# Optimization experiments

Hardware: AMD Instinct MI355X
Metric: run time of the kernel (lower is better)

## Reference

```python
import jax, jax.numpy as jnp
import numpy as np

B, S, D_IN = 2, 2048, 1024
H, DA, DH = 16, 64, 64          # num_heads, attention_dim, head_dim (linear_hidden_dim)
EMBED = 1024
KSIZE = 1


def causal_conv1d(x_bsc, w):
    """x_bsc: (B,S,Cin); w: (Cout,Cin,K). Left-pad K-1 -> causal. Returns (B,Cout,S)."""
    k = w.shape[-1]
    x_bcs = jnp.transpose(x_bsc, (0, 2, 1))
    x_bcs = jnp.pad(x_bcs, ((0, 0), (0, 0), (k - 1, 0)))
    return jax.lax.conv_general_dilated(
        x_bcs, w, window_strides=(1,), padding='VALID',
        dimension_numbers=('NCH', 'OIH', 'NCH'))


def setup_inputs() -> dict:
    key = jax.random.key(0)
    ks = jax.random.split(key, 7)
    x = jax.random.normal(ks[0], (B, S, D_IN), dtype=jnp.float32)
    # causal mask: 1 where attended, 0 where masked (masked_fill where ==0)
    attn_mask = jnp.tril(jnp.ones((S, S), dtype=jnp.int32))[None, None]  # (1,1,S,S)
    wq = 0.02 * jax.random.normal(ks[1], (H * DA, D_IN, KSIZE), dtype=jnp.float32)
    wk = 0.02 * jax.random.normal(ks[2], (H * DA, D_IN, KSIZE), dtype=jnp.float32)
    wv = 0.02 * jax.random.normal(ks[3], (H * DH, D_IN, KSIZE), dtype=jnp.float32)
    w_out = 0.02 * jax.random.normal(ks[4], (EMBED, H * DH), dtype=jnp.float32)
    b_out = 0.02 * jax.random.normal(ks[5], (EMBED,), dtype=jnp.float32)
    return {"x": x, "attn_mask": attn_mask, "wq": wq, "wk": wk, "wv": wv,
            "w_out": w_out, "b_out": b_out}


def reference(x, attn_mask, wq, wk, wv, w_out, b_out):
    b, s, _ = x.shape
    scale = DH ** (-0.5)  # NOTE: torch code scales by head_dim, not attention_dim
    q = causal_conv1d(x, wq)  # (B, H*DA, S)
    k = causal_conv1d(x, wk)  # (B, H*DA, S)
    v = causal_conv1d(x, wv)  # (B, H*DH, S)
    q = q.reshape(b, H, DA, s).transpose(0, 1, 3, 2)  # (B,H,S,DA)
    k = k.reshape(b, H, DA, s).transpose(0, 1, 3, 2)
    v = v.reshape(b, H, DH, s).transpose(0, 1, 3, 2)  # (B,H,S,DH)
    scores = scale * jnp.einsum('bhnd,bhmd->bhnm', q, k)
    scores = jnp.where(attn_mask == 0, -jnp.inf, scores)
    probs = jax.nn.softmax(scores, axis=-1)
    context = jnp.einsum('bhnm,bhmd->bhnd', probs, v)  # (B,H,S,DH)
    context = context.transpose(0, 2, 1, 3).reshape(b, s, H * DH)
    return context @ w_out.T + b_out
```

## Files before the change

kernel.cpp:

```cpp
#include <hip/hip_runtime.h>
#include <math.h>


typedef __bf16 bf16;
typedef __bf16 bf16x8 __attribute__((ext_vector_type(8)));
typedef __bf16 bf16x4 __attribute__((ext_vector_type(4)));
typedef float  f32x4  __attribute__((ext_vector_type(4)));

#define MFMA16(a, b, c) __builtin_amdgcn_mfma_f32_16x16x32_bf16((a), (b), (c), 0, 0, 0)

__device__ __forceinline__ void gll16(const void* g, void* l) {
    __builtin_amdgcn_global_load_lds(
        (__attribute__((address_space(1))) unsigned int*)g,
        (__attribute__((address_space(3))) unsigned int*)l, 16, 0, 0);
}

__global__ __launch_bounds__(256) void cvt_all_kernel(
    const float* __restrict__ x,  const float* __restrict__ wq,
    const float* __restrict__ wk, const float* __restrict__ wv,
    const float* __restrict__ wo,
    bf16* __restrict__ xb,  bf16* __restrict__ wqb, bf16* __restrict__ wkb,
    bf16* __restrict__ wvb, bf16* __restrict__ wob)
{
    #pragma unroll
    for (int k = 0; k < 4; k++) {
        const int blk = blockIdx.x * 4 + k;
        const float* src; bf16* dst; int off; float scale = 1.f;
        if (blk < 4096)      { src = x;  dst = xb;  off = blk * 1024; }
        else if (blk < 5120) { src = wq; dst = wqb; off = (blk - 4096) * 1024;
                               scale = 0.18033688011112042f; }
        else if (blk < 6144) { src = wk; dst = wkb; off = (blk - 5120) * 1024; }
        else if (blk < 7168) { src = wv; dst = wvb; off = (blk - 6144) * 1024; }
        else                 { src = wo; dst = wob; off = (blk - 7168) * 1024; }
        const int i = off + threadIdx.x * 4;
        f32x4 v = *(const f32x4*)(src + i);
        bf16x4 o;
        o[0] = (bf16)(v[0] * scale); o[1] = (bf16)(v[1] * scale);
        o[2] = (bf16)(v[2] * scale); o[3] = (bf16)(v[3] * scale);
        *(bf16x4*)(dst + i) = o;
    }
}

__global__ __launch_bounds__(256, 3) void qkv_mfma_kernel(
    const bf16* __restrict__ xb, const bf16* __restrict__ wqb,
    const bf16* __restrict__ wkb, const bf16* __restrict__ wvb,
    bf16* __restrict__ Qb, bf16* __restrict__ Kb, bf16* __restrict__ Vtb)
{
    __shared__ bf16 As[2][128 * 32];
    __shared__ bf16 Bs[2][128 * 32];
    const int lin = blockIdx.x + 32 * blockIdx.y;
    const int xcd = lin & 7, lid = lin >> 3;
    const int rem = xcd * 96 + lid;
    const int mt = rem & 31;
    const int nt = rem >> 5;
    const int which = nt >> 3;
    const bf16* Wm = (which == 0) ? wqb : (which == 1) ? wkb : wvb;

    const int t = threadIdx.x;
    const int w = t >> 6, lane = t & 63, quad = lane >> 4, l16 = lane & 15;
    const int wm = (w >> 1) * 64, wn = (w & 1) * 64;
    const int srow = lane >> 2;
    const int scol = (lane & 3) * 8;

    const bf16* Ab = xb + ((size_t)(mt * 128) + srow) * 1024 + scol;
    const bf16* Bb = Wm + ((size_t)((nt & 7) * 128) + srow) * 1024 + scol;

    f32x4 acc[4][4];
    #pragma unroll
    for (int i = 0; i < 4; i++)
        #pragma unroll
        for (int j = 0; j < 4; j++)
            #pragma unroll
            for (int r = 0; r < 4; r++) acc[i][j][r] = 0.f;

    gll16(Ab + (size_t)(w * 16) * 1024,       As[0] + w * 512);
    gll16(Ab + (size_t)((w + 4) * 16) * 1024, As[0] + (w + 4) * 512);
    gll16(Bb + (size_t)(w * 16) * 1024,       Bs[0] + w * 512);
    gll16(Bb + (size_t)((w + 4) * 16) * 1024, Bs[0] + (w + 4) * 512);

    for (int it = 0; it < 32; it++) {
        const int cur = it & 1, nxt = cur ^ 1;
        __syncthreads();
        if (it < 31) {
            const int kn = it * 32 + 32;
            gll16(Ab + (size_t)(w * 16) * 1024 + kn,       As[nxt] + w * 512);
            gll16(Ab + (size_t)((w + 4) * 16) * 1024 + kn, As[nxt] + (w + 4) * 512);
            gll16(Bb + (size_t)(w * 16) * 1024 + kn,       Bs[nxt] + w * 512);
            gll16(Bb + (size_t)((w + 4) * 16) * 1024 + kn, Bs[nxt] + (w + 4) * 512);
        }
        bf16x8 af[4], bfr[4];
        #pragma unroll
        for (int i = 0; i < 4; i++)
            af[i] = *(const bf16x8*)&As[cur][(wm + i * 16 + l16) * 32 + quad * 8];
        #pragma unroll
        for (int j = 0; j < 4; j++)
            bfr[j] = *(const bf16x8*)&Bs[cur][(wn + j * 16 + l16) * 32 + quad * 8];
        #pragma unroll
        for (int i = 0; i < 4; i++)
            #pragma unroll
            for (int j = 0; j < 4; j++)
                acc[i][j] = MFMA16(af[i], bfr[j], acc[i][j]);
    }

    const int nbase = (nt & 7) * 128 + wn;
    if (which == 2) {
        #pragma unroll
        for (int i = 0; i < 4; i++) {
            const int m0 = mt * 128 + wm + i * 16 + quad * 4;
            const int bb = m0 >> 11, s0 = m0 & 2047;
            #pragma unroll
            for (int j = 0; j < 4; j++) {
                const int n = nbase + j * 16 + l16;
                const int h = n >> 6, d = n & 63;
                bf16x4 pk;
                #pragma unroll
                for (int r = 0; r < 4; r++) pk[r] = (bf16)acc[i][j][r];
                *(bf16x4*)&Vtb[(((size_t)(bb * 16 + h)) * 64 + d) * 2048 + s0] = pk;
            }
        }
    } else {
        bf16* Out = (which == 0) ? Qb : Kb;
        #pragma unroll
        for (int i = 0; i < 4; i++) {
            #pragma unroll
            for (int r = 0; r < 4; r++) {
                const int m = mt * 128 + wm + i * 16 + quad * 4 + r;
                const int bb = m >> 11, s = m & 2047;
                #pragma unroll
                for (int j = 0; j < 4; j++) {
                    const int n = nbase + j * 16 + l16;
                    const int h = n >> 6, d = n & 63;
                    Out[(((size_t)(bb * 16 + h)) * 2048 + s) * 64 + d] =
                        (bf16)acc[i][j][r];
                }
            }
        }
    }
}

__global__ __launch_bounds__(256, 2) void attn_mfma_kernel(
    const bf16* __restrict__ Qb, const bf16* __restrict__ Kb,
    const bf16* __restrict__ Vtb, bf16* __restrict__ ctxb)
{
    __shared__ bf16 Ks[2][128 * 64];
    __shared__ bf16 Vts[2][64 * 128];
    __shared__ bf16 Pl[4][16 * 128];

    const int id = blockIdx.x;
    const int bh = id & 31;
    const int pr = id >> 5;
    const int qa = pr, qb = 31 - pr;
    const int h = bh & 15, b = bh >> 4;
    const int t = threadIdx.x;
    const int w = t >> 6, lane = t & 63, quad = lane >> 4, l16 = lane & 15;

    const size_t hb = (size_t)(b * 16 + h);
    const bf16* Qh = Qb + hb * (2048 * 64);
    const bf16* Kh = Kb + hb * (2048 * 64);
    const bf16* Vh = Vtb + hb * (64 * 2048);

    bf16x8 qf0[2], qf1[2];
    {
        const bf16* Qr0 = Qh + (size_t)(qa * 64 + w * 16 + l16) * 64;
        qf0[0] = *(const bf16x8*)(Qr0 + quad * 8);
        qf0[1] = *(const bf16x8*)(Qr0 + 32 + quad * 8);
        const bf16* Qr1 = Qh + (size_t)(qb * 64 + w * 16 + l16) * 64;
        qf1[0] = *(const bf16x8*)(Qr1 + quad * 8);
        qf1[1] = *(const bf16x8*)(Qr1 + 32 + quad * 8);
    }

    bf16x8 ones;
    #pragma unroll
    for (int i = 0; i < 8; i++) ones[i] = (bf16)1.0f;

    f32x4 o0[4], o1[4], l0, l1;
    #pragma unroll
    for (int r = 0; r < 4; r++) { l0[r] = 0.f; l1[r] = 0.f; }
    #pragma unroll
    for (int dt = 0; dt < 4; dt++)
        #pragma unroll
        for (int r = 0; r < 4; r++) { o0[dt][r] = 0.f; o1[dt][r] = 0.f; }

    const int ksr = lane >> 3, ksc = lane & 7;
    const int vsr = lane >> 4, vsc = lane & 15;

    #define STAGE(ktv, buf)                                                   \
        {                                                                     \
            _Pragma("unroll")                                                 \
            for (int j = 0; j < 4; j++) {                                     \
                const int c = 4 * w + j;                                      \
                const int kr = c * 8 + ksr;                                   \
                gll16(Kh + (size_t)((ktv) * 128 + kr) * 64 +                  \
                          ((ksc ^ (kr & 7)) * 8),                             \
                      Ks[buf] + c * 512);                                     \
                const int vr = c * 4 + vsr;                                   \
                gll16(Vh + (size_t)vr * 2048 + (ktv) * 128 +                  \
                          ((vsc ^ (vr & 15)) * 8),                            \
                      Vts[buf] + c * 512);                                    \
            }                                                                 \
        }

    #define ITER(qt64, ktv, diag, qfv, oacc, lacc, cur)                       \
        {                                                                     \
            f32x4 sacc[8];                                                    \
            __builtin_amdgcn_s_setprio(1);                                    \
            _Pragma("unroll")                                                 \
            for (int tt = 0; tt < 8; tt++) {                                  \
                _Pragma("unroll")                                             \
                for (int r = 0; r < 4; r++) sacc[tt][r] = 0.f;                \
                const int krow = tt * 16 + l16;                               \
                bf16x8 kf0 = *(const bf16x8*)&Ks[cur][krow * 64 +             \
                                 ((quad)     ^ (krow & 7)) * 8];              \
                bf16x8 kf1 = *(const bf16x8*)&Ks[cur][krow * 64 +             \
                                 ((quad + 4) ^ (krow & 7)) * 8];              \
                sacc[tt] = MFMA16(kf0, (qfv)[0], sacc[tt]);                   \
                sacc[tt] = MFMA16(kf1, (qfv)[1], sacc[tt]);                   \
            }                                                                 \
            __builtin_amdgcn_s_setprio(0);                                    \
            const int qrow = (qt64) * 64 + w * 16 + l16;                      \
            _Pragma("unroll")                                                 \
            for (int tt = 0; tt < 8; tt++) {                                  \
                bf16x4 pk;                                                    \
                _Pragma("unroll")                                             \
                for (int r = 0; r < 4; r++) {                                 \
                    float p = __builtin_amdgcn_exp2f(sacc[tt][r]);            \
                    if ((diag) && ((ktv) * 128 + tt * 16 + quad * 4 + r) > qrow) \
                        p = 0.f;                                              \
                    pk[r] = (bf16)p;                                          \
                }                                                             \
                const int cs = (tt * 2 + (quad >> 1)) ^ l16;                  \
                *(bf16x4*)&Pl[w][l16 * 128 + cs * 8 + (quad & 1) * 4] = pk;   \
            }                                                                 \
            bf16x8 ap[4];                                                     \
            __builtin_amdgcn_s_setprio(1);                                    \
            _Pragma("unroll")                                                 \
            for (int u = 0; u < 4; u++) {                                     \
                ap[u] = *(const bf16x8*)&Pl[w][l16 * 128 +                    \
                             ((quad + 4 * u) ^ l16) * 8];                     \
                (lacc) = MFMA16(ap[u], ones, (lacc));                         \
            }                                                                 \
            _Pragma("unroll")                                                 \
            for (int dt = 0; dt < 4; dt++) {                                  \
                const int drow = dt * 16 + l16;                               \
                _Pragma("unroll")                                             \
                for (int u = 0; u < 4; u++) {                                 \
                    bf16x8 bv = *(const bf16x8*)&Vts[cur][drow * 128 +        \
                                     ((4 * u + quad) ^ (drow & 15)) * 8];     \
                    (oacc)[dt] = MFMA16(ap[u], bv, (oacc)[dt]);               \
                }                                                             \
            }                                                                 \
            __builtin_amdgcn_s_setprio(0);                                    \
        }

    const int na = (qa >> 1) + 1;
    STAGE(0, 0);

    for (int v = 0; v < 17; v++) {
        const int cur = v & 1, nxt = cur ^ 1;
        __syncthreads();
        if (v < 16) {
            const int vn = v + 1;
            const int ktn = (vn < na) ? vn : vn - na;
            STAGE(ktn, nxt);
        }
        if (v < na) {
            ITER(qa, v, (v == na - 1), qf0, o0, l0, cur);
        } else {
            const int kt = v - na;
            ITER(qb, kt, (v == 16), qf1, o1, l1, cur);
        }
    }
    #undef STAGE
    #undef ITER

    #pragma unroll
    for (int r = 0; r < 4; r++) {
        const float inv0 = 1.f / l0[r];
        const int s0 = qa * 64 + w * 16 + quad * 4 + r;
        const float inv1 = 1.f / l1[r];
        const int s1 = qb * 64 + w * 16 + quad * 4 + r;
        #pragma unroll
        for (int dt = 0; dt < 4; dt++) {
            ctxb[((size_t)(b * 2048 + s0)) * 1024 + h * 64 + dt * 16 + l16] =
                (bf16)(o0[dt][r] * inv0);
            ctxb[((size_t)(b * 2048 + s1)) * 1024 + h * 64 + dt * 16 + l16] =
                (bf16)(o1[dt][r] * inv1);
        }
    }
}

__global__ __launch_bounds__(256, 3) void oproj_mfma_kernel(
    const bf16* __restrict__ ctxb, const bf16* __restrict__ wob,
    const float* __restrict__ b_out, float* __restrict__ out)
{
    __shared__ bf16 As[2][64 * 64];
    __shared__ bf16 Bs[2][128 * 64];
    const int mt = blockIdx.x;
    const int nt = blockIdx.y;
    const int t = threadIdx.x;
    const int w = t >> 6, lane = t & 63, quad = lane >> 4, l16 = lane & 15;
    const int srow8 = lane >> 3;
    const int scg = ((lane & 7) ^ srow8) * 8;

    const int wrow = (w >> 1) * 32;
    const int wcol = (w & 1) * 64;

    const bf16* Ab = ctxb + (size_t)(mt * 64) * 1024;
    const bf16* Bb = wob + (size_t)(nt * 128) * 1024;

    f32x4 acc[2][4];
    #pragma unroll
    for (int i = 0; i < 2; i++)
        #pragma unroll
        for (int j = 0; j < 4; j++)
            #pragma unroll
            for (int r = 0; r < 4; r++) acc[i][j][r] = 0.f;

    #define OSTG(buf, kk)                                                     \
        {                                                                     \
            gll16(Ab + (size_t)(w * 8 + srow8) * 1024 + (kk) + scg,           \
                  As[buf] + w * 512);                                         \
            gll16(Ab + (size_t)((w + 4) * 8 + srow8) * 1024 + (kk) + scg,     \
                  As[buf] + (w + 4) * 512);                                   \
            _Pragma("unroll")                                                 \
            for (int c = 0; c < 4; c++) {                                     \
                const int ch = w + 4 * c;                                     \
                gll16(Bb + (size_t)(ch * 8 + srow8) * 1024 + (kk) + scg,      \
                      Bs[buf] + ch * 512);                                    \
            }                                                                 \
        }

    OSTG(0, 0);

    for (int it = 0; it < 16; it++) {
        const int cur = it & 1, nxt = cur ^ 1;
        __syncthreads();
        if (it < 15) { OSTG(nxt, it * 64 + 64); }
        bf16x8 af[2][2], bfv[4][2];
        #pragma unroll
        for (int i = 0; i < 2; i++) {
            const int ro = wrow + i * 16 + l16;
            af[i][0] = *(const bf16x8*)&As[cur][ro * 64 + ((quad)     ^ (ro & 7)) * 8];
            af[i][1] = *(const bf16x8*)&As[cur][ro * 64 + ((quad + 4) ^ (ro & 7)) * 8];
        }
        #pragma unroll
        for (int j = 0; j < 4; j++) {
            const int ro = wcol + j * 16 + l16;
            bfv[j][0] = *(const bf16x8*)&Bs[cur][ro * 64 + ((quad)     ^ (ro & 7)) * 8];
            bfv[j][1] = *(const bf16x8*)&Bs[cur][ro * 64 + ((quad + 4) ^ (ro & 7)) * 8];
        }
        #pragma unroll
        for (int i = 0; i < 2; i++)
            #pragma unroll
            for (int j = 0; j < 4; j++) {
                acc[i][j] = MFMA16(af[i][0], bfv[j][0], acc[i][j]);
                acc[i][j] = MFMA16(af[i][1], bfv[j][1], acc[i][j]);
            }
    }
    #undef OSTG

    #pragma unroll
    for (int i = 0; i < 2; i++)
        #pragma unroll
        for (int j = 0; j < 4; j++)
            #pragma unroll
            for (int r = 0; r < 4; r++) {
                const int m = mt * 64 + wrow + i * 16 + quad * 4 + r;
                const int n = nt * 128 + wcol + j * 16 + l16;
                out[(size_t)m * 1024 + n] = acc[i][j][r] + b_out[n];
            }
}

extern "C" void kernel_launch(void* const* d_in, const int* in_sizes, int n_in,
                              void* d_out, int out_size, void* d_ws, size_t ws_size,
                              hipStream_t stream)
{
    const float* x     = (const float*)d_in[0];
    const float* wq    = (const float*)d_in[2];
    const float* wk    = (const float*)d_in[3];
    const float* wv    = (const float*)d_in[4];
    const float* w_out = (const float*)d_in[5];
    const float* b_out = (const float*)d_in[6];
    float* out = (float*)d_out;

    char* ws = (char*)d_ws;
    bf16* xb   = (bf16*)(ws);
    bf16* wqb  = (bf16*)(ws + (8u  << 20));
    bf16* wkb  = (bf16*)(ws + (10u << 20));
    bf16* wvb  = (bf16*)(ws + (12u << 20));
    bf16* wob  = (bf16*)(ws + (14u << 20));
    bf16* Qb   = (bf16*)(ws + (16u << 20));
    bf16* Kb   = (bf16*)(ws + (24u << 20));
    bf16* Vtb  = (bf16*)(ws + (32u << 20));
    bf16* ctxb = (bf16*)(ws + (40u << 20));

    cvt_all_kernel<<<2048, 256, 0, stream>>>(x, wq, wk, wv, w_out,
                                             xb, wqb, wkb, wvb, wob);
    qkv_mfma_kernel<<<dim3(32, 24), 256, 0, stream>>>(xb, wqb, wkb, wvb, Qb, Kb, Vtb);
    attn_mfma_kernel<<<512, 256, 0, stream>>>(Qb, Kb, Vtb, ctxb);
    oproj_mfma_kernel<<<dim3(64, 8), 256, 0, stream>>>(ctxb, wob, b_out, out);
}
```

Baseline: 179.3 us.

## Split attention waves across paired query tiles and swizzle QKV GEMM LDS

```diff
diff --git a/kernel.cpp b/kernel.cpp
--- a/kernel.cpp
+++ b/kernel.cpp
@@ -60,10 +60,11 @@
     const int w = t >> 6, lane = t & 63, quad = lane >> 4, l16 = lane & 15;
     const int wm = (w >> 1) * 64, wn = (w & 1) * 64;
     const int srow = lane >> 2;
-    const int scol = (lane & 3) * 8;
-
-    const bf16* Ab = xb + ((size_t)(mt * 128) + srow) * 1024 + scol;
-    const bf16* Bb = Wm + ((size_t)((nt & 7) * 128) + srow) * 1024 + scol;
+    const int scol = ((lane & 3) ^ ((lane >> 3) & 3)) * 8;
+    const int gx = (l16 >> 1) & 3;
+
+    const bf16* Ab = xb + ((size_t)(mt * 128) + srow) * 1024;
+    const bf16* Bb = Wm + ((size_t)((nt & 7) * 128) + srow) * 1024;
 
     f32x4 acc[4][4];
     #pragma unroll
@@ -73,28 +74,30 @@
             #pragma unroll
             for (int r = 0; r < 4; r++) acc[i][j][r] = 0.f;
 
-    gll16(Ab + (size_t)(w * 16) * 1024,       As[0] + w * 512);
-    gll16(Ab + (size_t)((w + 4) * 16) * 1024, As[0] + (w + 4) * 512);
-    gll16(Bb + (size_t)(w * 16) * 1024,       Bs[0] + w * 512);
-    gll16(Bb + (size_t)((w + 4) * 16) * 1024, Bs[0] + (w + 4) * 512);
+    gll16(Ab + (size_t)(w * 16) * 1024 + scol,       As[0] + w * 512);
+    gll16(Ab + (size_t)((w + 4) * 16) * 1024 + scol, As[0] + (w + 4) * 512);
+    gll16(Bb + (size_t)(w * 16) * 1024 + scol,       Bs[0] + w * 512);
+    gll16(Bb + (size_t)((w + 4) * 16) * 1024 + scol, Bs[0] + (w + 4) * 512);
 
     for (int it = 0; it < 32; it++) {
         const int cur = it & 1, nxt = cur ^ 1;
         __syncthreads();
         if (it < 31) {
             const int kn = it * 32 + 32;
-            gll16(Ab + (size_t)(w * 16) * 1024 + kn,       As[nxt] + w * 512);
-            gll16(Ab + (size_t)((w + 4) * 16) * 1024 + kn, As[nxt] + (w + 4) * 512);
-            gll16(Bb + (size_t)(w * 16) * 1024 + kn,       Bs[nxt] + w * 512);
-            gll16(Bb + (size_t)((w + 4) * 16) * 1024 + kn, Bs[nxt] + (w + 4) * 512);
+            gll16(Ab + (size_t)(w * 16) * 1024 + kn + scol,       As[nxt] + w * 512);
+            gll16(Ab + (size_t)((w + 4) * 16) * 1024 + kn + scol, As[nxt] + (w + 4) * 512);
+            gll16(Bb + (size_t)(w * 16) * 1024 + kn + scol,       Bs[nxt] + w * 512);
+            gll16(Bb + (size_t)((w + 4) * 16) * 1024 + kn + scol, Bs[nxt] + (w + 4) * 512);
         }
         bf16x8 af[4], bfr[4];
         #pragma unroll
         for (int i = 0; i < 4; i++)
-            af[i] = *(const bf16x8*)&As[cur][(wm + i * 16 + l16) * 32 + quad * 8];
+            af[i] = *(const bf16x8*)&As[cur][(wm + i * 16 + l16) * 32 +
+                                             (quad ^ gx) * 8];
         #pragma unroll
         for (int j = 0; j < 4; j++)
-            bfr[j] = *(const bf16x8*)&Bs[cur][(wn + j * 16 + l16) * 32 + quad * 8];
+            bfr[j] = *(const bf16x8*)&Bs[cur][(wn + j * 16 + l16) * 32 +
+                                              (quad ^ gx) * 8];
         #pragma unroll
         for (int i = 0; i < 4; i++)
             #pragma unroll
@@ -142,49 +145,55 @@
     const bf16* __restrict__ Qb, const bf16* __restrict__ Kb,
     const bf16* __restrict__ Vtb, bf16* __restrict__ ctxb)
 {
-    __shared__ bf16 Ks[2][128 * 64];
+    __shared__ bf16 Ks[128 * 64];
     __shared__ bf16 Vts[2][64 * 128];
-    __shared__ bf16 Pl[4][16 * 128];
+    __shared__ bf16 Pl[4][32 * 128];
 
     const int id = blockIdx.x;
     const int bh = id & 31;
     const int pr = id >> 5;
-    const int qa = pr, qb = 31 - pr;
     const int h = bh & 15, b = bh >> 4;
     const int t = threadIdx.x;
     const int w = t >> 6, lane = t & 63, quad = lane >> 4, l16 = lane & 15;
+
+    const int na = (pr >> 1) + 1;
+    const int nb = 17 - na;
+    const int tile = (w < 2) ? pr : (31 - pr);
+    const int nme  = (w < 2) ? na : nb;
+    const int rbase = tile * 64 + (w & 1) * 32;
 
     const size_t hb = (size_t)(b * 16 + h);
     const bf16* Qh = Qb + hb * (2048 * 64);
     const bf16* Kh = Kb + hb * (2048 * 64);
     const bf16* Vh = Vtb + hb * (64 * 2048);
 
-    bf16x8 qf0[2], qf1[2];
-    {
-        const bf16* Qr0 = Qh + (size_t)(qa * 64 + w * 16 + l16) * 64;
-        qf0[0] = *(const bf16x8*)(Qr0 + quad * 8);
-        qf0[1] = *(const bf16x8*)(Qr0 + 32 + quad * 8);
-        const bf16* Qr1 = Qh + (size_t)(qb * 64 + w * 16 + l16) * 64;
-        qf1[0] = *(const bf16x8*)(Qr1 + quad * 8);
-        qf1[1] = *(const bf16x8*)(Qr1 + 32 + quad * 8);
+    bf16x8 qf[2][2];
+    #pragma unroll
+    for (int s = 0; s < 2; s++) {
+        const bf16* Qr = Qh + (size_t)(rbase + s * 16 + l16) * 64;
+        qf[s][0] = *(const bf16x8*)(Qr + quad * 8);
+        qf[s][1] = *(const bf16x8*)(Qr + 32 + quad * 8);
     }
 
     bf16x8 ones;
     #pragma unroll
     for (int i = 0; i < 8; i++) ones[i] = (bf16)1.0f;
 
-    f32x4 o0[4], o1[4], l0, l1;
-    #pragma unroll
-    for (int r = 0; r < 4; r++) { l0[r] = 0.f; l1[r] = 0.f; }
-    #pragma unroll
-    for (int dt = 0; dt < 4; dt++)
-        #pragma unroll
-        for (int r = 0; r < 4; r++) { o0[dt][r] = 0.f; o1[dt][r] = 0.f; }
+    f32x4 o[2][4], l[2];
+    #pragma unroll
+    for (int s = 0; s < 2; s++) {
+        #pragma unroll
+        for (int r = 0; r < 4; r++) l[s][r] = 0.f;
+        #pragma unroll
+        for (int dt = 0; dt < 4; dt++)
+            #pragma unroll
+            for (int r = 0; r < 4; r++) o[s][dt][r] = 0.f;
+    }
 
     const int ksr = lane >> 3, ksc = lane & 7;
     const int vsr = lane >> 4, vsc = lane & 15;
 
-    #define STAGE(ktv, buf)                                                   \
+    #define STAGE_K(ktv)                                                      \
         {                                                                     \
             _Pragma("unroll")                                                 \
             for (int j = 0; j < 4; j++) {                                     \
@@ -192,7 +201,14 @@
                 const int kr = c * 8 + ksr;                                   \
                 gll16(Kh + (size_t)((ktv) * 128 + kr) * 64 +                  \
                           ((ksc ^ (kr & 7)) * 8),                             \
-                      Ks[buf] + c * 512);                                     \
+                      Ks + c * 512);                                          \
+            }                                                                 \
+        }
+    #define STAGE_V(ktv, buf)                                                 \
+        {                                                                     \
+            _Pragma("unroll")                                                 \
+            for (int j = 0; j < 4; j++) {                                     \
+                const int c = 4 * w + j;                                      \
                 const int vr = c * 4 + vsr;                                   \
                 gll16(Vh + (size_t)vr * 2048 + (ktv) * 128 +                  \
                           ((vsc ^ (vr & 15)) * 8),                            \
@@ -200,93 +216,95 @@
             }                                                                 \
         }
 
-    #define ITER(qt64, ktv, diag, qfv, oacc, lacc, cur)                       \
-        {                                                                     \
-            f32x4 sacc[8];                                                    \
-            __builtin_amdgcn_s_setprio(1);                                    \
-            _Pragma("unroll")                                                 \
-            for (int tt = 0; tt < 8; tt++) {                                  \
-                _Pragma("unroll")                                             \
-                for (int r = 0; r < 4; r++) sacc[tt][r] = 0.f;                \
-                const int krow = tt * 16 + l16;                               \
-                bf16x8 kf0 = *(const bf16x8*)&Ks[cur][krow * 64 +             \
-                                 ((quad)     ^ (krow & 7)) * 8];              \
-                bf16x8 kf1 = *(const bf16x8*)&Ks[cur][krow * 64 +             \
-                                 ((quad + 4) ^ (krow & 7)) * 8];              \
-                sacc[tt] = MFMA16(kf0, (qfv)[0], sacc[tt]);                   \
-                sacc[tt] = MFMA16(kf1, (qfv)[1], sacc[tt]);                   \
-            }                                                                 \
-            __builtin_amdgcn_s_setprio(0);                                    \
-            const int qrow = (qt64) * 64 + w * 16 + l16;                      \
-            _Pragma("unroll")                                                 \
-            for (int tt = 0; tt < 8; tt++) {                                  \
-                bf16x4 pk;                                                    \
-                _Pragma("unroll")                                             \
-                for (int r = 0; r < 4; r++) {                                 \
-                    float p = __builtin_amdgcn_exp2f(sacc[tt][r]);            \
-                    if ((diag) && ((ktv) * 128 + tt * 16 + quad * 4 + r) > qrow) \
-                        p = 0.f;                                              \
-                    pk[r] = (bf16)p;                                          \
-                }                                                             \
-                const int cs = (tt * 2 + (quad >> 1)) ^ l16;                  \
-                *(bf16x4*)&Pl[w][l16 * 128 + cs * 8 + (quad & 1) * 4] = pk;   \
-            }                                                                 \
-            bf16x8 ap[4];                                                     \
-            __builtin_amdgcn_s_setprio(1);                                    \
-            _Pragma("unroll")                                                 \
-            for (int u = 0; u < 4; u++) {                                     \
-                ap[u] = *(const bf16x8*)&Pl[w][l16 * 128 +                    \
-                             ((quad + 4 * u) ^ l16) * 8];                     \
-                (lacc) = MFMA16(ap[u], ones, (lacc));                         \
-            }                                                                 \
-            _Pragma("unroll")                                                 \
-            for (int dt = 0; dt < 4; dt++) {                                  \
-                const int drow = dt * 16 + l16;                               \
-                _Pragma("unroll")                                             \
-                for (int u = 0; u < 4; u++) {                                 \
-                    bf16x8 bv = *(const bf16x8*)&Vts[cur][drow * 128 +        \
-                                     ((4 * u + quad) ^ (drow & 15)) * 8];     \
-                    (oacc)[dt] = MFMA16(ap[u], bv, (oacc)[dt]);               \
-                }                                                             \
-            }                                                                 \
-            __builtin_amdgcn_s_setprio(0);                                    \
-        }
-
-    const int na = (qa >> 1) + 1;
-    STAGE(0, 0);
-
-    for (int v = 0; v < 17; v++) {
-        const int cur = v & 1, nxt = cur ^ 1;
+    STAGE_K(0); STAGE_V(0, 0);
+    __syncthreads();
+
+    for (int v = 0; v < nb; v++) {
+        const int cur = v & 1;
+        const bool act  = (v < nme);
+        const bool diag = act && (v == nme - 1);
+
+        f32x4 sacc[2][8];
+        if (act) {
+            __builtin_amdgcn_s_setprio(1);
+            #pragma unroll
+            for (int tt = 0; tt < 8; tt++) {
+                const int krow = tt * 16 + l16;
+                bf16x8 kf0 = *(const bf16x8*)&Ks[krow * 64 +
+                                 ((quad)     ^ (krow & 7)) * 8];
+                bf16x8 kf1 = *(const bf16x8*)&Ks[krow * 64 +
+                                 ((quad + 4) ^ (krow & 7)) * 8];
+                #pragma unroll
+                for (int s = 0; s < 2; s++) {
+                    #pragma unroll
+                    for (int r = 0; r < 4; r++) sacc[s][tt][r] = 0.f;
+                    sacc[s][tt] = MFMA16(kf0, qf[s][0], sacc[s][tt]);
+                    sacc[s][tt] = MFMA16(kf1, qf[s][1], sacc[s][tt]);
+                }
+            }
+            __builtin_amdgcn_s_setprio(0);
+        }
         __syncthreads();
-        if (v < 16) {
-            const int vn = v + 1;
-            const int ktn = (vn < na) ? vn : vn - na;
-            STAGE(ktn, nxt);
-        }
-        if (v < na) {
-            ITER(qa, v, (v == na - 1), qf0, o0, l0, cur);
-        } else {
-            const int kt = v - na;
-            ITER(qb, kt, (v == 16), qf1, o1, l1, cur);
-        }
-    }
-    #undef STAGE
-    #undef ITER
-
-    #pragma unroll
-    for (int r = 0; r < 4; r++) {
-        const float inv0 = 1.f / l0[r];
-        const int s0 = qa * 64 + w * 16 + quad * 4 + r;
-        const float inv1 = 1.f / l1[r];
-        const int s1 = qb * 64 + w * 16 + quad * 4 + r;
-        #pragma unroll
-        for (int dt = 0; dt < 4; dt++) {
-            ctxb[((size_t)(b * 2048 + s0)) * 1024 + h * 64 + dt * 16 + l16] =
-                (bf16)(o0[dt][r] * inv0);
-            ctxb[((size_t)(b * 2048 + s1)) * 1024 + h * 64 + dt * 16 + l16] =
-                (bf16)(o1[dt][r] * inv1);
-        }
-    }
+        if (v + 1 < nb) { STAGE_K(v + 1); STAGE_V(v + 1, cur ^ 1); }
+        if (act) {
+            #pragma unroll
+            for (int s = 0; s < 2; s++) {
+                const int qrow = rbase + s * 16 + l16;
+                #pragma unroll
+                for (int tt = 0; tt < 8; tt++) {
+                    bf16x4 pk;
+                    #pragma unroll
+                    for (int r = 0; r < 4; r++) {
+                        float p = __builtin_amdgcn_exp2f(sacc[s][tt][r]);
+                        if (diag && (v * 128 + tt * 16 + quad * 4 + r) > qrow)
+                            p = 0.f;
+                        pk[r] = (bf16)p;
+                    }
+                    const int cs = (tt * 2 + (quad >> 1)) ^ l16;
+                    *(bf16x4*)&Pl[w][s * 2048 + l16 * 128 + cs * 8 +
+                                     (quad & 1) * 4] = pk;
+                }
+            }
+            bf16x8 ap[2][4];
+            __builtin_amdgcn_s_setprio(1);
+            #pragma unroll
+            for (int s = 0; s < 2; s++)
+                #pragma unroll
+                for (int u = 0; u < 4; u++) {
+                    ap[s][u] = *(const bf16x8*)&Pl[w][s * 2048 + l16 * 128 +
+                                   ((quad + 4 * u) ^ l16) * 8];
+                    l[s] = MFMA16(ap[s][u], ones, l[s]);
+                }
+            #pragma unroll
+            for (int dt = 0; dt < 4; dt++) {
+                const int drow = dt * 16 + l16;
+                #pragma unroll
+                for (int u = 0; u < 4; u++) {
+                    bf16x8 bv = *(const bf16x8*)&Vts[cur][drow * 128 +
+                                     ((4 * u + quad) ^ (drow & 15)) * 8];
+                    o[0][dt] = MFMA16(ap[0][u], bv, o[0][dt]);
+                    o[1][dt] = MFMA16(ap[1][u], bv, o[1][dt]);
+                }
+            }
+            __builtin_amdgcn_s_setprio(0);
+        }
+        __syncthreads();
+    }
+    #undef STAGE_K
+    #undef STAGE_V
+
+    #pragma unroll
+    for (int s = 0; s < 2; s++)
+        #pragma unroll
+        for (int r = 0; r < 4; r++) {
+            const float inv = 1.f / l[s][r];
+            const int srow = rbase + s * 16 + quad * 4 + r;
+            #pragma unroll
+            for (int dt = 0; dt < 4; dt++) {
+                ctxb[((size_t)(b * 2048 + srow)) * 1024 + h * 64 + dt * 16 + l16] =
+                    (bf16)(o[s][dt][r] * inv);
+            }
+        }
 }
 
 __global__ __launch_bounds__(256, 3) void oproj_mfma_kernel(
```

After: 184.1 us. 2.7% more time.
